# Kernel optimization log

Hardware: AMD Instinct MI355X
Metric: run time of the kernel (lower is better)

## Reference

```python
import jax, jax.numpy as jnp
import numpy as np

B, NQ, NK = 4, 512, 512
DQ, DK, DV = 512, 512, 512
H = 128
MASK_VAL = -1e6


def setup_inputs() -> dict:
    key = jax.random.key(0)
    kq, kk, kv, kwq, kwk, kwv, kl = jax.random.split(key, 7)
    queries = jax.random.normal(kq, (B, NQ, DQ), dtype=jnp.float32)
    keys = jax.random.normal(kk, (B, NK, DK), dtype=jnp.float32)
    values = jax.random.normal(kv, (B, NK, DV), dtype=jnp.float32)
    # Dense(num_hiddens, use_bias=False) weights, Glorot-ish scale
    Wq = jax.random.normal(kwq, (DQ, H), dtype=jnp.float32) / np.sqrt(DQ)
    Wk = jax.random.normal(kwk, (DK, H), dtype=jnp.float32) / np.sqrt(DK)
    Wv = jax.random.normal(kwv, (H,), dtype=jnp.float32) / np.sqrt(H)  # Dense(1) as a vector
    valid_lens = jax.random.randint(kl, (B,), 1, NK + 1, dtype=jnp.int32)
    return {"queries": queries, "keys": keys, "values": values,
            "Wq": Wq, "Wk": Wk, "Wv": Wv, "valid_lens": valid_lens}


def reference(queries, keys, values, Wq, Wk, Wv, valid_lens):
    # Project queries/keys to hidden dim
    q = jnp.einsum('bqd,dh->bqh', queries, Wq)   # [B,NQ,H]
    k = jnp.einsum('bkd,dh->bkh', keys, Wk)      # [B,NK,H]
    # Broadcast add + tanh -> [B,NQ,NK,H] (the big intermediate)
    features = jnp.tanh(q[:, :, None, :] + k[:, None, :, :])
    # W_v reduces hidden dim to a scalar score
    scores = jnp.einsum('bqkh,h->bqk', features, Wv)  # [B,NQ,NK]
    # masked softmax over keys: positions >= valid_len get -1e6 (as in d2l sequence_mask)
    mask = jnp.arange(NK, dtype=jnp.int32)[None, None, :] < valid_lens[:, None, None]
    scores = jnp.where(mask, scores, MASK_VAL)
    attn = jax.nn.softmax(scores, axis=-1)
    # dropout rate 0.0 -> identity
    return jnp.einsum('bqk,bkv->bqv', attn, values)  # [B,NQ,DV]
```

## Files before the change

kernel.cpp:

```cpp
#include <hip/hip_runtime.h>

#ifndef __has_builtin
#define __has_builtin(x) 0
#endif

#if __has_builtin(__builtin_amdgcn_exp2f)
#define EXP2F(x) __builtin_amdgcn_exp2f(x)
#else
#define EXP2F(x) exp2f(x)
#endif
#if __has_builtin(__builtin_amdgcn_rcpf)
#define RCPF(x) __builtin_amdgcn_rcpf(x)
#else
#define RCPF(x) (1.0f / (x))
#endif

static constexpr int NB = 4, NQ = 512, NK = 512, DD = 512, HH = 128, DV = 512;
static constexpr float MASKV = -1e6f;
static constexpr float C2LOG2E = 2.885390081777926814f;

typedef __attribute__((ext_vector_type(8))) short bf16x8;
typedef __attribute__((ext_vector_type(4))) float f32x4;

__device__ __forceinline__ unsigned short f2bf(float x) {
  unsigned int u = __float_as_uint(x);
  u += 0x7FFFu + ((u >> 16) & 1u);
  return (unsigned short)(u >> 16);
}
__device__ __forceinline__ float bf2f(unsigned short h) {
  return __uint_as_float(((unsigned int)h) << 16);
}
__device__ __forceinline__ void split2(float x, unsigned short& hi, unsigned short& lo) {
  hi = f2bf(x);
  lo = f2bf(x - bf2f(hi));
}

__global__ __launch_bounds__(256) void proj_mfma_vt_kernel(
    const float* __restrict__ queries, const float* __restrict__ keys,
    const float* __restrict__ Wq, const float* __restrict__ Wk,
    const float* __restrict__ values, const int* __restrict__ valid_lens,
    float* __restrict__ eq, float* __restrict__ ekT4,
    unsigned short* __restrict__ Vt) {
  __shared__ __align__(16) unsigned short smem_us[20736];
  const int bid = blockIdx.x;
  const int t = threadIdx.x;

  if (bid < 256) {
    const int row0 = bid << 4;
    const bool isK = row0 >= 2048;
    int b = 0, kloc = 0;
    const float* inb;
    const float* W;
    if (isK) {
      const int local = row0 - 2048;
      b = local >> 9;
      kloc = local & 511;
      if (kloc >= valid_lens[b]) return;
      inb = keys + (size_t)local * DD;
      W = Wk;
    } else {
      inb = queries + (size_t)row0 * DD;
      W = Wq;
    }

    unsigned short* Ah = smem_us;
    unsigned short* Al = smem_us + 1152;
    unsigned short* Wh = smem_us + 2304;
    unsigned short* Wl = smem_us + 11520;

    const int w = t >> 6, l = t & 63;
    const int lm = l & 15;
    const int lk8 = (l >> 4) << 3;

    const f32x4 z = {0.f, 0.f, 0.f, 0.f};
    f32x4 acc[2] = {z, z};

    const int ar = t >> 4, ac4 = (t & 15) << 2;
    const int wh = t & 127, wkg = (t >> 7) << 5;

    for (int kt = 0; kt < 8; ++kt) {
      const int k0 = kt << 6;
      {
        const float4 v = *reinterpret_cast<const float4*>(inb + (size_t)ar * DD + k0 + ac4);
        unsigned short h0, h1, h2, h3, l0, l1, l2, l3;
        split2(v.x, h0, l0); split2(v.y, h1, l1);
        split2(v.z, h2, l2); split2(v.w, h3, l3);
        uint2 ph = make_uint2((unsigned int)h0 | ((unsigned int)h1 << 16),
                              (unsigned int)h2 | ((unsigned int)h3 << 16));
        uint2 pl = make_uint2((unsigned int)l0 | ((unsigned int)l1 << 16),
                              (unsigned int)l2 | ((unsigned int)l3 << 16));
        *reinterpret_cast<uint2*>(Ah + ar * 72 + ac4) = ph;
        *reinterpret_cast<uint2*>(Al + ar * 72 + ac4) = pl;
      }
      {
        unsigned int hw[16], lw[16];
#pragma unroll
        for (int i = 0; i < 16; ++i) {
          const float w0 = W[(size_t)(k0 + wkg + 2 * i) * HH + wh];
          const float w1 = W[(size_t)(k0 + wkg + 2 * i + 1) * HH + wh];
          unsigned short a0, a1, b0, b1;
          split2(w0, a0, b0); split2(w1, a1, b1);
          hw[i] = (unsigned int)a0 | ((unsigned int)a1 << 16);
          lw[i] = (unsigned int)b0 | ((unsigned int)b1 << 16);
        }
        unsigned int* dh = reinterpret_cast<unsigned int*>(Wh + wh * 72 + wkg);
        unsigned int* dl = reinterpret_cast<unsigned int*>(Wl + wh * 72 + wkg);
#pragma unroll
        for (int i = 0; i < 4; ++i) {
          *reinterpret_cast<uint4*>(dh + 4 * i) =
              make_uint4(hw[4 * i], hw[4 * i + 1], hw[4 * i + 2], hw[4 * i + 3]);
          *reinterpret_cast<uint4*>(dl + 4 * i) =
              make_uint4(lw[4 * i], lw[4 * i + 1], lw[4 * i + 2], lw[4 * i + 3]);
        }
      }
      __syncthreads();

#pragma unroll
      for (int kh = 0; kh < 2; ++kh) {
        const int ko = lk8 + (kh << 5);
        const bf16x8 ah = *reinterpret_cast<const bf16x8*>(Ah + lm * 72 + ko);
        const bf16x8 al = *reinterpret_cast<const bf16x8*>(Al + lm * 72 + ko);
#pragma unroll
        for (int c = 0; c < 2; ++c) {
          const int hrow = (w << 5) + (c << 4) + lm;
          const bf16x8 bh = *reinterpret_cast<const bf16x8*>(Wh + hrow * 72 + ko);
          const bf16x8 bl = *reinterpret_cast<const bf16x8*>(Wl + hrow * 72 + ko);
          acc[c] = __builtin_amdgcn_mfma_f32_16x16x32_bf16(ah, bh, acc[c], 0, 0, 0);
          acc[c] = __builtin_amdgcn_mfma_f32_16x16x32_bf16(al, bh, acc[c], 0, 0, 0);
          acc[c] = __builtin_amdgcn_mfma_f32_16x16x32_bf16(ah, bl, acc[c], 0, 0, 0);
        }
      }
      __syncthreads();
    }

    const int rb = (l >> 4) << 2;
    if (!isK) {
#pragma unroll
      for (int c = 0; c < 2; ++c) {
        const int h = (w << 5) + (c << 4) + lm;
#pragma unroll
        for (int j = 0; j < 4; ++j)
          eq[(size_t)(row0 + rb + j) * HH + h] = EXP2F(acc[c][j] * C2LOG2E);
      }
    } else {
      float* tile = reinterpret_cast<float*>(smem_us);
#pragma unroll
      for (int c = 0; c < 2; ++c) {
        const int h = (w << 5) + (c << 4) + lm;
#pragma unroll
        for (int j = 0; j < 4; ++j)
          tile[(rb + j) * 132 + h] = EXP2F(acc[c][j] * C2LOG2E);
      }
      __syncthreads();
#pragma unroll
      for (int i = 0; i < 2; ++i) {
        const int idx = t + (i << 8);
        const int k = idx & 15, h4 = idx >> 4;
        const float4 v = *reinterpret_cast<const float4*>(tile + k * 132 + (h4 << 2));
        *reinterpret_cast<float4*>(
            ekT4 + ((((size_t)b * 32 + h4) << 9) + kloc + k) * 4) = v;
      }
    }
  } else {
    unsigned short (*tl)[72] = reinterpret_cast<unsigned short (*)[72]>(smem_us);
    const int vb = bid - 256;
    const int b = vb >> 6;
    const int tile = vb & 63;
    const int k0 = (tile >> 3) << 6;
    const int v0 = (tile & 7) << 6;
    const int kr = t >> 4, c4 = (t & 15) << 2;
#pragma unroll
    for (int pp = 0; pp < 4; ++pp) {
      const int k = kr + (pp << 4);
      const float4 v = *reinterpret_cast<const float4*>(
          values + ((size_t)(b * NK + k0 + k)) * DV + v0 + c4);
      tl[k][c4 + 0] = f2bf(v.x); tl[k][c4 + 1] = f2bf(v.y);
      tl[k][c4 + 2] = f2bf(v.z); tl[k][c4 + 3] = f2bf(v.w);
    }
    __syncthreads();
    const int vr = t >> 2, seg = t & 3;
    unsigned int pk[8];
#pragma unroll
    for (int i = 0; i < 8; ++i) {
      const int kc = (seg << 4) + (i << 1);
      pk[i] = (unsigned int)tl[kc][vr] | ((unsigned int)tl[kc + 1][vr] << 16);
    }
    unsigned short* dst = Vt + ((size_t)(b * NK + v0 + vr)) * NK + k0 + (seg << 4);
    *reinterpret_cast<uint4*>(dst) = make_uint4(pk[0], pk[1], pk[2], pk[3]);
    *reinterpret_cast<uint4*>(dst + 8) = make_uint4(pk[4], pk[5], pk[6], pk[7]);
  }
}

__global__ __launch_bounds__(1024) void scores_softmax_kernel(
    const float* __restrict__ eq, const float* __restrict__ ekT4,
    const float* __restrict__ Wv, const int* __restrict__ valid_lens,
    unsigned short* __restrict__ attnQ) {
  const int b = blockIdx.x >> 7;
  const int q0 = (blockIdx.x & 127) << 2;
  const int t = threadIdx.x;
  const int kk = t & 511, hh = t >> 9;

  __shared__ __align__(16) float qs[4][HH];
  __shared__ __align__(16) float wv[HH];
  __shared__ __align__(16) float scp[2][4][NK];

  if (t < 512) {
    qs[t >> 7][t & 127] = eq[((size_t)(b * NQ + q0 + (t >> 7))) * HH + (t & 127)];
  } else if (t < 640) {
    wv[t - 512] = Wv[t - 512];
  }
  __syncthreads();

  const int vl = valid_lens[b];
  float s0 = 0.f, s1 = 0.f, s2 = 0.f, s3 = 0.f;

  if (kk < vl) {
    const float* ekb4 = ekT4 + (((size_t)(b * 32 + hh * 16) << 9) + kk) * 4;
#pragma unroll 8
    for (int i = 0; i < 16; ++i) {
      const float4 e4 = *reinterpret_cast<const float4*>(ekb4 + ((size_t)i << 11));
      const int h = (hh * 16 + i) << 2;
      const float4 w4 = *reinterpret_cast<const float4*>(&wv[h]);
      const float4 qa = *reinterpret_cast<const float4*>(&qs[0][h]);
      const float4 qb = *reinterpret_cast<const float4*>(&qs[1][h]);
      const float4 qc = *reinterpret_cast<const float4*>(&qs[2][h]);
      const float4 qd = *reinterpret_cast<const float4*>(&qs[3][h]);
      float u, v, num, r;
      u = fmaf(qa.x, e4.x, 1.f); v = fmaf(qa.y, e4.y, 1.f);
      num = fmaf(w4.x, v, w4.y * u); r = RCPF(u * v); s0 = fmaf(num, r, s0);
      u = fmaf(qa.z, e4.z, 1.f); v = fmaf(qa.w, e4.w, 1.f);
      num = fmaf(w4.z, v, w4.w * u); r = RCPF(u * v); s0 = fmaf(num, r, s0);
      u = fmaf(qb.x, e4.x, 1.f); v = fmaf(qb.y, e4.y, 1.f);
      num = fmaf(w4.x, v, w4.y * u); r = RCPF(u * v); s1 = fmaf(num, r, s1);
      u = fmaf(qb.z, e4.z, 1.f); v = fmaf(qb.w, e4.w, 1.f);
      num = fmaf(w4.z, v, w4.w * u); r = RCPF(u * v); s1 = fmaf(num, r, s1);
      u = fmaf(qc.x, e4.x, 1.f); v = fmaf(qc.y, e4.y, 1.f);
      num = fmaf(w4.x, v, w4.y * u); r = RCPF(u * v); s2 = fmaf(num, r, s2);
      u = fmaf(qc.z, e4.z, 1.f); v = fmaf(qc.w, e4.w, 1.f);
      num = fmaf(w4.z, v, w4.w * u); r = RCPF(u * v); s2 = fmaf(num, r, s2);
      u = fmaf(qd.x, e4.x, 1.f); v = fmaf(qd.y, e4.y, 1.f);
      num = fmaf(w4.x, v, w4.y * u); r = RCPF(u * v); s3 = fmaf(num, r, s3);
      u = fmaf(qd.z, e4.z, 1.f); v = fmaf(qd.w, e4.w, 1.f);
      num = fmaf(w4.z, v, w4.w * u); r = RCPF(u * v); s3 = fmaf(num, r, s3);
    }
  }
  scp[hh][0][kk] = s0;
  scp[hh][1][kk] = s1;
  scp[hh][2][kk] = s2;
  scp[hh][3][kk] = s3;
  __syncthreads();

  if (t < 256) {
    const int w = t >> 6, l = t & 63;
    float v[8];
#pragma unroll
    for (int j = 0; j < 8; ++j) {
      const int k = l + (j << 6);
      const float sv = scp[0][w][k] + scp[1][w][k];
      v[j] = (k < vl) ? (-2.f * sv) : MASKV;
    }
    float m = v[0];
#pragma unroll
    for (int j = 1; j < 8; ++j) m = fmaxf(m, v[j]);
#pragma unroll
    for (int off = 32; off > 0; off >>= 1) m = fmaxf(m, __shfl_xor(m, off, 64));
    float p[8], sum = 0.f;
#pragma unroll
    for (int j = 0; j < 8; ++j) {
      p[j] = __expf(v[j] - m);
      sum += p[j];
    }
#pragma unroll
    for (int off = 32; off > 0; off >>= 1) sum += __shfl_xor(sum, off, 64);
    const float inv = RCPF(sum);
#pragma unroll
    for (int j = 0; j < 8; ++j) scp[0][w][l + (j << 6)] = p[j] * inv;
  }
  __syncthreads();

  if (t < 512) {
#pragma unroll
    for (int j = 0; j < 4; ++j)
      attnQ[((size_t)(b * NQ + q0 + j)) * NK + t] = f2bf(scp[0][j][t]);
  }
}

__global__ __launch_bounds__(256) void pv_mfma_kernel(
    const unsigned short* __restrict__ attnQ, const unsigned short* __restrict__ Vt,
    const int* __restrict__ valid_lens, float* __restrict__ out) {
  const int bid = blockIdx.x;
  const int b = bid & 3;
  const int tile = bid >> 2;
  const int q0 = (tile >> 3) << 6;
  const int v0 = (tile & 7) << 6;

  __shared__ __align__(16) unsigned short Als[64 * 72];
  __shared__ __align__(16) unsigned short Bls[64 * 72];

  const int t = threadIdx.x;
  const int w = t >> 6, l = t & 63;
  const int wq = w >> 1, wv = w & 1;
  const int lm = l & 15;
  const int lk = (l >> 4) << 3;

  const f32x4 z = {0.f, 0.f, 0.f, 0.f};
  f32x4 acc[2][2] = {{z, z}, {z, z}};

  const int vl = valid_lens[b];
  const int nkt = (vl + 31) >> 5;

  const int sq = t >> 2, seg = t & 3;
  const unsigned short* arow = attnQ + ((size_t)(b * NQ + q0 + sq)) * NK;
  const unsigned short* brow = Vt + ((size_t)(b * NK + v0 + sq)) * NK;
  unsigned short* alds = &Als[sq * 72 + (seg << 3)];
  unsigned short* blds = &Bls[sq * 72 + (seg << 3)];

  for (int kt = 0; kt < nkt; ++kt) {
    const int k0 = kt << 5;
    *reinterpret_cast<bf16x8*>(alds) =
        *reinterpret_cast<const bf16x8*>(arow + k0 + (seg << 3));
    *reinterpret_cast<bf16x8*>(blds) =
        *reinterpret_cast<const bf16x8*>(brow + k0 + (seg << 3));
    __syncthreads();

    bf16x8 af[2], bfr[2];
#pragma unroll
    for (int mq = 0; mq < 2; ++mq)
      af[mq] = *reinterpret_cast<const bf16x8*>(
          &Als[(wq * 32 + mq * 16 + lm) * 72 + lk]);
#pragma unroll
    for (int nv = 0; nv < 2; ++nv)
      bfr[nv] = *reinterpret_cast<const bf16x8*>(
          &Bls[(wv * 32 + nv * 16 + lm) * 72 + lk]);
#pragma unroll
    for (int mq = 0; mq < 2; ++mq)
#pragma unroll
      for (int nv = 0; nv < 2; ++nv)
        acc[mq][nv] = __builtin_amdgcn_mfma_f32_16x16x32_bf16(
            af[mq], bfr[nv], acc[mq][nv], 0, 0, 0);
    __syncthreads();
  }

  const int rbase = (l >> 4) << 2;
#pragma unroll
  for (int mq = 0; mq < 2; ++mq) {
#pragma unroll
    for (int nv = 0; nv < 2; ++nv) {
      const int qg = q0 + wq * 32 + mq * 16 + rbase;
      const int vg = v0 + wv * 32 + nv * 16 + lm;
#pragma unroll
      for (int j = 0; j < 4; ++j)
        out[((size_t)(b * NQ + qg + j)) * DV + vg] = acc[mq][nv][j];
    }
  }
}

extern "C" void kernel_launch(void* const* d_in, const int* in_sizes, int n_in,
                              void* d_out, int out_size, void* d_ws, size_t ws_size,
                              hipStream_t stream) {
  (void)in_sizes; (void)n_in; (void)out_size; (void)ws_size;
  const float* queries = (const float*)d_in[0];
  const float* keys    = (const float*)d_in[1];
  const float* values  = (const float*)d_in[2];
  const float* Wq      = (const float*)d_in[3];
  const float* Wk      = (const float*)d_in[4];
  const float* Wv      = (const float*)d_in[5];
  const int*   vlens   = (const int*)d_in[6];
  float* out = (float*)d_out;
  float* ws = (float*)d_ws;

  float* eq   = ws;
  float* ekT4 = ws + 262144;
  unsigned short* attnQ = (unsigned short*)(ws + 524288);
  unsigned short* Vt    = (unsigned short*)(ws + 1048576);

  proj_mfma_vt_kernel<<<512, 256, 0, stream>>>(queries, keys, Wq, Wk, values,
                                               vlens, eq, ekT4, Vt);
  scores_softmax_kernel<<<512, 1024, 0, stream>>>(eq, ekT4, Wv, vlens, attnQ);
  pv_mfma_kernel<<<256, 256, 0, stream>>>(attnQ, Vt, vlens, out);
}
```

Baseline: 42.20 us.

## Re-split score and PV kernels into smaller blocks for more parallelism

The scores kernel now gives each 512-thread block 2 queries instead of 4, with each thread covering the full hidden dimension for one key, so the cross-thread partial-sum merge goes away. It launches twice as many blocks. The PV MFMA kernel uses 64x32 output tiles instead of 64x64, also doubling its block count. The intent is better occupancy across CUs for these small grids, at the cost of less reuse of k-projection and attention loads per block and more redundant global traffic.

```diff
diff --git a/kernel.cpp b/kernel.cpp
--- a/kernel.cpp
+++ b/kernel.cpp
@@ -191,40 +191,37 @@
   }
 }
 
-__global__ __launch_bounds__(1024) void scores_softmax_kernel(
+__global__ __launch_bounds__(512) void scores_softmax_kernel(
     const float* __restrict__ eq, const float* __restrict__ ekT4,
     const float* __restrict__ Wv, const int* __restrict__ valid_lens,
     unsigned short* __restrict__ attnQ) {
-  const int b = blockIdx.x >> 7;
-  const int q0 = (blockIdx.x & 127) << 2;
+  const int b = blockIdx.x & 3;
+  const int q0 = (blockIdx.x >> 2) << 1;
   const int t = threadIdx.x;
-  const int kk = t & 511, hh = t >> 9;
-
-  __shared__ __align__(16) float qs[4][HH];
+
+  __shared__ __align__(16) float qs[2][HH];
   __shared__ __align__(16) float wv[HH];
-  __shared__ __align__(16) float scp[2][4][NK];
-
-  if (t < 512) {
+  __shared__ __align__(16) float scp[2][NK];
+
+  if (t < 256) {
     qs[t >> 7][t & 127] = eq[((size_t)(b * NQ + q0 + (t >> 7))) * HH + (t & 127)];
-  } else if (t < 640) {
-    wv[t - 512] = Wv[t - 512];
+  } else if (t < 384) {
+    wv[t - 256] = Wv[t - 256];
   }
   __syncthreads();
 
   const int vl = valid_lens[b];
-  float s0 = 0.f, s1 = 0.f, s2 = 0.f, s3 = 0.f;
-
-  if (kk < vl) {
-    const float* ekb4 = ekT4 + (((size_t)(b * 32 + hh * 16) << 9) + kk) * 4;
+  float s0 = 0.f, s1 = 0.f;
+
+  if (t < vl) {
+    const float* ekb4 = ekT4 + ((((size_t)b * 32) << 9) + t) * 4;
 #pragma unroll 8
-    for (int i = 0; i < 16; ++i) {
+    for (int i = 0; i < 32; ++i) {
       const float4 e4 = *reinterpret_cast<const float4*>(ekb4 + ((size_t)i << 11));
-      const int h = (hh * 16 + i) << 2;
+      const int h = i << 2;
       const float4 w4 = *reinterpret_cast<const float4*>(&wv[h]);
       const float4 qa = *reinterpret_cast<const float4*>(&qs[0][h]);
       const float4 qb = *reinterpret_cast<const float4*>(&qs[1][h]);
-      const float4 qc = *reinterpret_cast<const float4*>(&qs[2][h]);
-      const float4 qd = *reinterpret_cast<const float4*>(&qs[3][h]);
       float u, v, num, r;
       u = fmaf(qa.x, e4.x, 1.f); v = fmaf(qa.y, e4.y, 1.f);
       num = fmaf(w4.x, v, w4.y * u); r = RCPF(u * v); s0 = fmaf(num, r, s0);
@@ -234,31 +231,18 @@
       num = fmaf(w4.x, v, w4.y * u); r = RCPF(u * v); s1 = fmaf(num, r, s1);
       u = fmaf(qb.z, e4.z, 1.f); v = fmaf(qb.w, e4.w, 1.f);
       num = fmaf(w4.z, v, w4.w * u); r = RCPF(u * v); s1 = fmaf(num, r, s1);
-      u = fmaf(qc.x, e4.x, 1.f); v = fmaf(qc.y, e4.y, 1.f);
-      num = fmaf(w4.x, v, w4.y * u); r = RCPF(u * v); s2 = fmaf(num, r, s2);
-      u = fmaf(qc.z, e4.z, 1.f); v = fmaf(qc.w, e4.w, 1.f);
-      num = fmaf(w4.z, v, w4.w * u); r = RCPF(u * v); s2 = fmaf(num, r, s2);
-      u = fmaf(qd.x, e4.x, 1.f); v = fmaf(qd.y, e4.y, 1.f);
-      num = fmaf(w4.x, v, w4.y * u); r = RCPF(u * v); s3 = fmaf(num, r, s3);
-      u = fmaf(qd.z, e4.z, 1.f); v = fmaf(qd.w, e4.w, 1.f);
-      num = fmaf(w4.z, v, w4.w * u); r = RCPF(u * v); s3 = fmaf(num, r, s3);
-    }
-  }
-  scp[hh][0][kk] = s0;
-  scp[hh][1][kk] = s1;
-  scp[hh][2][kk] = s2;
-  scp[hh][3][kk] = s3;
+    }
+  }
+  const bool act = (t < vl);
+  scp[0][t] = act ? (-2.f * s0) : MASKV;
+  scp[1][t] = act ? (-2.f * s1) : MASKV;
   __syncthreads();
 
-  if (t < 256) {
+  if (t < 128) {
     const int w = t >> 6, l = t & 63;
     float v[8];
 #pragma unroll
-    for (int j = 0; j < 8; ++j) {
-      const int k = l + (j << 6);
-      const float sv = scp[0][w][k] + scp[1][w][k];
-      v[j] = (k < vl) ? (-2.f * sv) : MASKV;
-    }
+    for (int j = 0; j < 8; ++j) v[j] = scp[w][l + (j << 6)];
     float m = v[0];
 #pragma unroll
     for (int j = 1; j < 8; ++j) m = fmaxf(m, v[j]);
@@ -274,15 +258,12 @@
     for (int off = 32; off > 0; off >>= 1) sum += __shfl_xor(sum, off, 64);
     const float inv = RCPF(sum);
 #pragma unroll
-    for (int j = 0; j < 8; ++j) scp[0][w][l + (j << 6)] = p[j] * inv;
+    for (int j = 0; j < 8; ++j) scp[w][l + (j << 6)] = p[j] * inv;
   }
   __syncthreads();
 
-  if (t < 512) {
-#pragma unroll
-    for (int j = 0; j < 4; ++j)
-      attnQ[((size_t)(b * NQ + q0 + j)) * NK + t] = f2bf(scp[0][j][t]);
-  }
+  attnQ[((size_t)(b * NQ + q0 + 0)) * NK + t] = f2bf(scp[0][t]);
+  attnQ[((size_t)(b * NQ + q0 + 1)) * NK + t] = f2bf(scp[1][t]);
 }
 
 __global__ __launch_bounds__(256) void pv_mfma_kernel(
@@ -291,67 +272,57 @@
   const int bid = blockIdx.x;
   const int b = bid & 3;
   const int tile = bid >> 2;
-  const int q0 = (tile >> 3) << 6;
-  const int v0 = (tile & 7) << 6;
-
-  __shared__ __align__(16) unsigned short Als[64 * 72];
-  __shared__ __align__(16) unsigned short Bls[64 * 72];
+  const int q0 = (tile >> 4) << 6;
+  const int v0 = (tile & 15) << 5;
+
+  __shared__ __align__(16) unsigned short Als[64 * 40];
+  __shared__ __align__(16) unsigned short Bls[32 * 40];
 
   const int t = threadIdx.x;
   const int w = t >> 6, l = t & 63;
-  const int wq = w >> 1, wv = w & 1;
   const int lm = l & 15;
   const int lk = (l >> 4) << 3;
 
   const f32x4 z = {0.f, 0.f, 0.f, 0.f};
-  f32x4 acc[2][2] = {{z, z}, {z, z}};
+  f32x4 acc[2] = {z, z};
 
   const int vl = valid_lens[b];
   const int nkt = (vl + 31) >> 5;
 
   const int sq = t >> 2, seg = t & 3;
   const unsigned short* arow = attnQ + ((size_t)(b * NQ + q0 + sq)) * NK;
-  const unsigned short* brow = Vt + ((size_t)(b * NK + v0 + sq)) * NK;
-  unsigned short* alds = &Als[sq * 72 + (seg << 3)];
-  unsigned short* blds = &Bls[sq * 72 + (seg << 3)];
+  unsigned short* alds = &Als[sq * 40 + (seg << 3)];
+  const unsigned short* brow = Vt + ((size_t)(b * NK + v0 + (t >> 2))) * NK;
+  unsigned short* blds = &Bls[(t >> 2) * 40 + (seg << 3)];
 
   for (int kt = 0; kt < nkt; ++kt) {
     const int k0 = kt << 5;
     *reinterpret_cast<bf16x8*>(alds) =
         *reinterpret_cast<const bf16x8*>(arow + k0 + (seg << 3));
-    *reinterpret_cast<bf16x8*>(blds) =
-        *reinterpret_cast<const bf16x8*>(brow + k0 + (seg << 3));
+    if (t < 128)
+      *reinterpret_cast<bf16x8*>(blds) =
+          *reinterpret_cast<const bf16x8*>(brow + k0 + (seg << 3));
     __syncthreads();
 
-    bf16x8 af[2], bfr[2];
-#pragma unroll
-    for (int mq = 0; mq < 2; ++mq)
-      af[mq] = *reinterpret_cast<const bf16x8*>(
-          &Als[(wq * 32 + mq * 16 + lm) * 72 + lk]);
-#pragma unroll
-    for (int nv = 0; nv < 2; ++nv)
-      bfr[nv] = *reinterpret_cast<const bf16x8*>(
-          &Bls[(wv * 32 + nv * 16 + lm) * 72 + lk]);
-#pragma unroll
-    for (int mq = 0; mq < 2; ++mq)
-#pragma unroll
-      for (int nv = 0; nv < 2; ++nv)
-        acc[mq][nv] = __builtin_amdgcn_mfma_f32_16x16x32_bf16(
-            af[mq], bfr[nv], acc[mq][nv], 0, 0, 0);
+    const bf16x8 af = *reinterpret_cast<const bf16x8*>(
+        &Als[((w << 4) + lm) * 40 + lk]);
+#pragma unroll
+    for (int nv = 0; nv < 2; ++nv) {
+      const bf16x8 bfr = *reinterpret_cast<const bf16x8*>(
+          &Bls[((nv << 4) + lm) * 40 + lk]);
+      acc[nv] = __builtin_amdgcn_mfma_f32_16x16x32_bf16(af, bfr, acc[nv], 0, 0, 0);
+    }
     __syncthreads();
   }
 
   const int rbase = (l >> 4) << 2;
 #pragma unroll
-  for (int mq = 0; mq < 2; ++mq) {
-#pragma unroll
-    for (int nv = 0; nv < 2; ++nv) {
-      const int qg = q0 + wq * 32 + mq * 16 + rbase;
-      const int vg = v0 + wv * 32 + nv * 16 + lm;
-#pragma unroll
-      for (int j = 0; j < 4; ++j)
-        out[((size_t)(b * NQ + qg + j)) * DV + vg] = acc[mq][nv][j];
-    }
+  for (int nv = 0; nv < 2; ++nv) {
+    const int qg = q0 + (w << 4) + rbase;
+    const int vg = v0 + (nv << 4) + lm;
+#pragma unroll
+    for (int j = 0; j < 4; ++j)
+      out[((size_t)(b * NQ + qg + j)) * DV + vg] = acc[nv][j];
   }
 }
 
@@ -376,6 +347,6 @@
 
   proj_mfma_vt_kernel<<<512, 256, 0, stream>>>(queries, keys, Wq, Wk, values,
                                                vlens, eq, ekT4, Vt);
-  scores_softmax_kernel<<<512, 1024, 0, stream>>>(eq, ekT4, Wv, vlens, attnQ);
-  pv_mfma_kernel<<<256, 256, 0, stream>>>(attnQ, Vt, vlens, out);
-}
+  scores_softmax_kernel<<<1024, 512, 0, stream>>>(eq, ekT4, Wv, vlens, attnQ);
+  pv_mfma_kernel<<<512, 256, 0, stream>>>(attnQ, Vt, vlens, out);
+}
```

New measurement: 50.33 us. 1.19x slower.
